# Kernel optimization log

Hardware: AMD Instinct MI355X
Metric: run time of the kernel (lower is better)

## Reference

```python
import jax, jax.numpy as jnp
import numpy as np

N_NODES = 100000
N_EDGES = 1600000
N_GRAPHS = 256
DIMS = [128, 128, 128, 128]  # gcn_layers_dim -> 3 GCNConv layers


def setup_inputs() -> dict:
    key = jax.random.key(0)
    ks = jax.random.split(key, 12)
    inp = {
        "x": jax.random.normal(ks[0], (N_NODES, DIMS[0]), jnp.float32),
        "edge_index": jax.random.randint(ks[1], (2, N_EDGES), 0, N_NODES),
        "edge_weight": jax.random.uniform(ks[2], (N_EDGES,), jnp.float32),
        "batch": jnp.sort(jax.random.randint(ks[3], (N_NODES,), 0, N_GRAPHS)),
    }
    for i in range(3):
        fan_in = DIMS[i]
        scale = 1.0 / np.sqrt(fan_in)
        inp[f"W{i+1}"] = jax.random.uniform(ks[4 + 2 * i], (DIMS[i], DIMS[i + 1]),
                                             jnp.float32, -scale, scale)
        inp[f"b{i+1}"] = jax.random.uniform(ks[5 + 2 * i], (DIMS[i + 1],),
                                             jnp.float32, -scale, scale)
    return inp


def reference(x, edge_index, edge_weight, batch, W1, b1, W2, b2, W3, b3):
    n = x.shape[0]
    # PyG GCNConv: add self-loops with weight 1, symmetric normalization.
    loop = jnp.arange(n)
    row = jnp.concatenate([edge_index[0], loop])  # source nodes
    col = jnp.concatenate([edge_index[1], loop])  # target nodes (aggregation index)
    w = jnp.concatenate([edge_weight, jnp.ones((n,), x.dtype)])
    deg = jax.ops.segment_sum(w, col, num_segments=n)
    dinv = jnp.where(deg > 0, jax.lax.rsqrt(deg), jnp.zeros_like(deg))
    norm = dinv[row] * w * dinv[col]  # [E+N]

    # global_mean_pool setup
    counts = jax.ops.segment_sum(jnp.ones((n,), x.dtype), batch,
                                 num_segments=N_GRAPHS)
    counts = jnp.maximum(counts, 1.0)[:, None]

    def gcn_conv(h, W, b):
        hl = h @ W                      # linear projection first (PyG order)
        msg = hl[row] * norm[:, None]   # gather + edge scaling
        out = jax.ops.segment_sum(msg, col, num_segments=n)  # scatter-add
        return out + b

    embeddings = []
    h = x
    for W, b in ((W1, b1), (W2, b2), (W3, b3)):
        h = gcn_conv(h, W, b)
        h = jax.nn.relu(h)              # relu_layers_index = [0,1,2]
        emb = jax.ops.segment_sum(h, batch, num_segments=N_GRAPHS) / counts
        embeddings.append(emb)          # gep = global_mean_pool
    return tuple(embeddings)
```

## Files before the change

kernel.cpp:

```cpp
#include <hip/hip_runtime.h>


typedef short short8 __attribute__((ext_vector_type(8)));
typedef float f32x4  __attribute__((ext_vector_type(4)));

__device__ inline unsigned pack_bf16x2(float a, float b) {
    unsigned ua = __float_as_uint(a);
    ua = (ua + 0x7FFFu + ((ua >> 16) & 1u)) >> 16;
    unsigned ub = __float_as_uint(b);
    ub = (ub + 0x7FFFu + ((ub >> 16) & 1u)) >> 16;
    return ua | (ub << 16);
}
__device__ inline ushort bf16_1(float a) {
    unsigned ua = __float_as_uint(a);
    return (ushort)((ua + 0x7FFFu + ((ua >> 16) & 1u)) >> 16);
}
__device__ inline float bf_lo(unsigned u) { return __uint_as_float(u << 16); }
__device__ inline float bf_hi(unsigned u) { return __uint_as_float(u & 0xFFFF0000u); }


template <bool F32IN>
__device__ __forceinline__ void gemm_tile(const void* __restrict__ Hin,
                                          const ushort* __restrict__ WbT,
                                          unsigned* __restrict__ O, int M,
                                          int bid, unsigned* sOut) {
    int lane = threadIdx.x & 63;
    int wv = threadIdx.x >> 6;
    int quad = lane >> 4;
    int mrow = lane & 15;
    int m0 = bid * 128 + wv * 32;
    int r0 = m0 + mrow;
    int r1 = r0 + 16;
    int r0c = r0 < M ? r0 : M - 1;
    int r1c = r1 < M ? r1 : M - 1;

    short8 a0[4], a1[4];
    if (F32IN) {
        const float* Hf = (const float*)Hin;
#pragma unroll
        for (int s = 0; s < 4; s++) {
            const float4* p0 = (const float4*)(Hf + (size_t)r0c * 128 + s * 32 + quad * 8);
            const float4* p1 = (const float4*)(Hf + (size_t)r1c * 128 + s * 32 + quad * 8);
            float4 f0 = p0[0], f1 = p0[1];
            float4 g0 = p1[0], g1 = p1[1];
            union { short8 s8; unsigned u[4]; } t0, t1;
            t0.u[0] = pack_bf16x2(f0.x, f0.y); t0.u[1] = pack_bf16x2(f0.z, f0.w);
            t0.u[2] = pack_bf16x2(f1.x, f1.y); t0.u[3] = pack_bf16x2(f1.z, f1.w);
            t1.u[0] = pack_bf16x2(g0.x, g0.y); t1.u[1] = pack_bf16x2(g0.z, g0.w);
            t1.u[2] = pack_bf16x2(g1.x, g1.y); t1.u[3] = pack_bf16x2(g1.z, g1.w);
            a0[s] = t0.s8; a1[s] = t1.s8;
        }
    } else {
        const unsigned* Hb = (const unsigned*)Hin;
#pragma unroll
        for (int s = 0; s < 4; s++) {
            a0[s] = *(const short8*)(Hb + (size_t)r0c * 64 + s * 16 + quad * 4);
            a1[s] = *(const short8*)(Hb + (size_t)r1c * 64 + s * 16 + quad * 4);
        }
    }
    f32x4 acc0[8], acc1[8];
#pragma unroll
    for (int t = 0; t < 8; t++) {
        acc0[t] = (f32x4){0.f, 0.f, 0.f, 0.f};
        acc1[t] = (f32x4){0.f, 0.f, 0.f, 0.f};
    }
#pragma unroll
    for (int s = 0; s < 4; s++) {
#pragma unroll
        for (int t = 0; t < 8; t++) {
            short8 b = *(const short8*)(WbT + (t * 16 + mrow) * 128 + s * 32 + quad * 8);
            acc0[t] = __builtin_amdgcn_mfma_f32_16x16x32_bf16(a0[s], b, acc0[t], 0, 0, 0);
            acc1[t] = __builtin_amdgcn_mfma_f32_16x16x32_bf16(a1[s], b, acc1[t], 0, 0, 0);
        }
    }
    ushort* so = (ushort*)(sOut + wv * 32 * 64);
#pragma unroll
    for (int t = 0; t < 8; t++) {
#pragma unroll
        for (int r = 0; r < 4; r++) {
            int lr = quad * 4 + r;
            int c = t * 16 + mrow;
            so[lr * 128 + c] = bf16_1(acc0[t][r]);
            so[(lr + 16) * 128 + c] = bf16_1(acc1[t][r]);
        }
    }
    __syncthreads();
    const unsigned* si = sOut + wv * 32 * 64;
#pragma unroll 8
    for (int r = 0; r < 32; r++) {
        int row = m0 + r;
        if (row < M) O[(size_t)row * 64 + lane] = si[r * 64 + lane];
    }
}

__device__ __forceinline__ void pool_tile(const unsigned* __restrict__ HB,
                                          const int* __restrict__ gb,
                                          float* __restrict__ outp, int g,
                                          float* part) {
    int lane = threadIdx.x & 63, w = threadIdx.x >> 6;
    int s = gb[g], e = gb[g + 1];
    float ax = 0.f, ay = 0.f;
    for (int i = s + w; i < e; i += 4) {
        unsigned u = HB[(size_t)i * 64 + lane];
        ax += bf_lo(u); ay += bf_hi(u);
    }
    part[w * 128 + lane * 2] = ax;
    part[w * 128 + lane * 2 + 1] = ay;
    __syncthreads();
    if (threadIdx.x < 128) {
        float sum = part[threadIdx.x] + part[128 + threadIdx.x]
                  + part[256 + threadIdx.x] + part[384 + threadIdx.x];
        float c = (float)(e - s);
        outp[g * 128 + threadIdx.x] = sum / fmaxf(c, 1.0f);
    }
}


__global__ void k_prep(int* __restrict__ cnt, int N, int* __restrict__ bsum,
                       const int* __restrict__ batch, int* __restrict__ gb, int G,
                       const float* __restrict__ W0, const float* __restrict__ W1,
                       const float* __restrict__ W2, ushort* __restrict__ WbT) {
    int id = blockIdx.x * blockDim.x + threadIdx.x;
    if (id < N) cnt[id] = 0;
    if (id < 128) bsum[id] = 0;
    if (id <= G) {
        int lo = 0, hi = N;
        while (lo < hi) { int mid = (lo + hi) >> 1; if (batch[mid] < id) lo = mid + 1; else hi = mid; }
        gb[id] = lo;
    }
    if (id < 3 * 16384) {
        int l = id >> 14;
        const float* W = (l == 0) ? W0 : ((l == 1) ? W1 : W2);
        int id2 = id & 16383;
        int n = id2 & 127, k = id2 >> 7;
        WbT[l * 16384 + n * 128 + k] = bf16_1(W[k * 128 + n]);
    }
}

__global__ __launch_bounds__(256) void k_phase1(const int* __restrict__ ei,
                                                int* __restrict__ cnt,
                                                int* __restrict__ epos, int E,
                                                const float* __restrict__ x,
                                                const ushort* __restrict__ WbT,
                                                unsigned* __restrict__ O, int M,
                                                int nbGemm) {
    __shared__ unsigned sBuf[8192];
    if (blockIdx.x < nbGemm) {
        gemm_tile<true>(x, WbT, O, M, blockIdx.x, sBuf);
        return;
    }
    int tid = (blockIdx.x - nbGemm) * 256 + threadIdx.x;
    if (tid < E) {
        int c = ei[E + tid];
        epos[tid] = atomicAdd(&cnt[c], 1);
    }
}

__global__ __launch_bounds__(1024) void k_scan1(const int* __restrict__ cnt,
                                                int* __restrict__ pre,
                                                int* __restrict__ bsum, int n) {
    __shared__ int wsum[16];
    int t = threadIdx.x, lane = t & 63, w = t >> 6;
    int i = blockIdx.x * 1024 + t;
    int v = (i < n) ? cnt[i] : 0;
    int x = v;
#pragma unroll
    for (int off = 1; off < 64; off <<= 1) {
        int y = __shfl_up(x, off, 64);
        if (lane >= off) x += y;
    }
    if (lane == 63) wsum[w] = x;
    __syncthreads();
    int woff = 0, tot = 0;
#pragma unroll
    for (int q = 0; q < 16; q++) { int s = wsum[q]; if (q < w) woff += s; tot += s; }
    if (i < n) pre[i] = woff + x - v;
    if (t == 0) bsum[blockIdx.x] = tot;
}

__global__ __launch_bounds__(256) void k_scatter(const int* __restrict__ ei,
                                                 const float* __restrict__ ew,
                                                 const int* __restrict__ pre,
                                                 const int* __restrict__ bsumRaw,
                                                 int* __restrict__ ptrv,
                                                 const int* __restrict__ epos,
                                                 int2* __restrict__ csr, int E, int N) {
    __shared__ int sRaw[256];
    __shared__ int sPre[256];
    __shared__ int sWt[4];
    int t = threadIdx.x;
    sRaw[t] = (t < 128) ? bsumRaw[t] : 0;
    __syncthreads();
    int lane = t & 63, w2 = t >> 6;
    int v = sRaw[t];
    int x = v;
#pragma unroll
    for (int off = 1; off < 64; off <<= 1) {
        int y = __shfl_up(x, off, 64);
        if (lane >= off) x += y;
    }
    if (lane == 63) sWt[w2] = x;
    __syncthreads();
    int base = 0;
#pragma unroll
    for (int q = 0; q < 4; q++) { if (q < w2) base += sWt[q]; }
    sPre[t] = base + x - v;
    __syncthreads();
    int e = blockIdx.x * 256 + t;
    if (e < N) ptrv[e] = pre[e] + sPre[e >> 10];
    if (e == 0) ptrv[N] = sWt[0] + sWt[1];
    if (e >= E) return;
    int r = ei[e];
    int c = ei[E + e];
    int2 mv; mv.x = r; mv.y = __float_as_int(ew[e]);
    csr[pre[c] + sPre[c >> 10] + epos[e]] = mv;
}

__global__ __launch_bounds__(256) void k_degdinv(const int2* __restrict__ csr,
                                                 const int* __restrict__ ptrv,
                                                 float* __restrict__ dinv, int N) {
    int node = blockIdx.x * 8 + (threadIdx.x >> 5);
    int j = threadIdx.x & 31;
    if (node >= N) return;
    int e0 = ptrv[node], e1 = ptrv[node + 1];
    float s = (j == 0) ? 1.0f : 0.0f;
    for (int e = e0 + j; e < e1; e += 32) s += __int_as_float(csr[e].y);
#pragma unroll
    for (int off = 1; off < 32; off <<= 1) s += __shfl_xor(s, off, 64);
    if (j == 0) dinv[node] = rsqrtf(s);
}

__global__ __launch_bounds__(256) void k_norm(int2* __restrict__ csr,
                                              const int* __restrict__ ptrv,
                                              const float* __restrict__ dinv, int N) {
    int node = blockIdx.x * 8 + (threadIdx.x >> 5);
    int j = threadIdx.x & 31;
    if (node >= N) return;
    float dc = dinv[node];
    int e0 = ptrv[node], e1 = ptrv[node + 1];
    for (int e = e0 + j; e < e1; e += 32) {
        int2 m = csr[e];
        m.y = __float_as_int(dinv[m.x] * __int_as_float(m.y) * dc);
        csr[e] = m;
    }
}

__global__ __launch_bounds__(256) void k_agg(const unsigned* __restrict__ HL,
                                             const int* __restrict__ ptr,
                                             const int2* __restrict__ csr,
                                             const float* __restrict__ dinv,
                                             const float* __restrict__ bias,
                                             unsigned* __restrict__ Hout, int M) {
    __shared__ int2 sM[4 * 64];
    int node = (int)((blockIdx.x * blockDim.x + threadIdx.x) >> 6);
    if (node >= M) return;
    int lane = threadIdx.x & 63;
    int half = lane >> 5;
    int q = lane & 31;
    int2* mbase = &sM[(threadIdx.x >> 6) * 64];
    int e0 = ptr[node], e1 = ptr[node + 1];
    int deg = e1 - e0;
    int nbv = deg < 64 ? deg : 64;
    if (lane < nbv) mbase[lane] = csr[e0 + lane];
    const uint2* HL2 = (const uint2*)HL;
    float di = dinv[node];
    float sn = (half == 0) ? di * di : 0.f;
    uint2 us = HL2[(size_t)node * 32 + q];
    float a0 = sn * bf_lo(us.x), a1 = sn * bf_hi(us.x);
    float a2 = sn * bf_lo(us.y), a3 = sn * bf_hi(us.y);
    int j = half;
    for (; j + 8 <= nbv; j += 8) {
        int2 m[4]; uint2 u[4];
#pragma unroll
        for (int t = 0; t < 4; t++) m[t] = mbase[j + 2 * t];
#pragma unroll
        for (int t = 0; t < 4; t++) u[t] = HL2[(size_t)m[t].x * 32 + q];
#pragma unroll
        for (int t = 0; t < 4; t++) {
            float nv = __int_as_float(m[t].y);
            a0 += nv * bf_lo(u[t].x); a1 += nv * bf_hi(u[t].x);
            a2 += nv * bf_lo(u[t].y); a3 += nv * bf_hi(u[t].y);
        }
    }
    for (; j < nbv; j += 2) {
        int2 m = mbase[j];
        uint2 u = HL2[(size_t)m.x * 32 + q];
        float nv = __int_as_float(m.y);
        a0 += nv * bf_lo(u.x); a1 += nv * bf_hi(u.x);
        a2 += nv * bf_lo(u.y); a3 += nv * bf_hi(u.y);
    }
    for (int e = e0 + 64 + half; e < e1; e += 2) {
        int2 m = csr[e];
        uint2 u = HL2[(size_t)m.x * 32 + q];
        float nv = __int_as_float(m.y);
        a0 += nv * bf_lo(u.x); a1 += nv * bf_hi(u.x);
        a2 += nv * bf_lo(u.y); a3 += nv * bf_hi(u.y);
    }
    a0 += __shfl_xor(a0, 32, 64);
    a1 += __shfl_xor(a1, 32, 64);
    a2 += __shfl_xor(a2, 32, 64);
    a3 += __shfl_xor(a3, 32, 64);
    float4 bv = ((const float4*)bias)[q];
    float r0 = fmaxf(a0 + bv.x, 0.f);
    float r1 = fmaxf(a1 + bv.y, 0.f);
    float r2 = fmaxf(a2 + bv.z, 0.f);
    float r3 = fmaxf(a3 + bv.w, 0.f);
    if (half == 0) {
        uint2 pv;
        pv.x = pack_bf16x2(r0, r1);
        pv.y = pack_bf16x2(r2, r3);
        ((uint2*)(Hout + (size_t)node * 64))[q] = pv;
    }
}

__global__ __launch_bounds__(256) void k_gemm_pool(const unsigned* __restrict__ Hb,
                                                   const ushort* __restrict__ WbT,
                                                   unsigned* __restrict__ O, int M,
                                                   const int* __restrict__ gb,
                                                   float* __restrict__ outp,
                                                   int nbGemm) {
    __shared__ unsigned sBuf[8192];
    if (blockIdx.x < nbGemm) {
        gemm_tile<false>(Hb, WbT, O, M, blockIdx.x, sBuf);
        return;
    }
    pool_tile(Hb, gb, outp, blockIdx.x - nbGemm, (float*)sBuf);
}

extern "C" void kernel_launch(void* const* d_in, const int* in_sizes, int n_in,
                              void* d_out, int out_size, void* d_ws, size_t ws_size,
                              hipStream_t stream) {
    const float* x     = (const float*)d_in[0];
    const int*   ei    = (const int*)d_in[1];
    const float* ew    = (const float*)d_in[2];
    const int*   batch = (const int*)d_in[3];
    const float* Wt[3] = {(const float*)d_in[4], (const float*)d_in[6], (const float*)d_in[8]};
    const float* bt[3] = {(const float*)d_in[5], (const float*)d_in[7], (const float*)d_in[9]};
    float* out = (float*)d_out;

    const int D = 128;
    const int N = in_sizes[0] / D;
    const int E = in_sizes[2];
    const int G = out_size / (3 * D);

    char* p = (char*)d_ws;
    auto alloc = [&](size_t bytes) {
        void* r = (void*)p;
        p += (bytes + 255) & ~(size_t)255;
        return r;
    };
    int*      cnt    = (int*)alloc((size_t)N * 4);
    int*      ptr    = (int*)alloc((size_t)(N + 1) * 4);
    int*      pre    = (int*)alloc((size_t)N * 4);
    int*      bsum   = (int*)alloc((size_t)128 * 4);
    int*      gb     = (int*)alloc((size_t)(G + 1) * 4);
    float*    dinv   = (float*)alloc((size_t)N * 4);
    ushort*   WbT    = (ushort*)alloc((size_t)3 * 16384 * 2);
    int2*     csr    = (int2*)alloc((size_t)E * 8);
    unsigned* bufHL  = (unsigned*)alloc((size_t)N * 64 * 4);
    unsigned* bufH   = (unsigned*)alloc((size_t)N * 64 * 4);
    int*      epos   = (int*)bufH;

    int nb = (N + 1023) / 1024;
    int nbGemm = (N + 127) / 128;
    int nbAtomic = (E + 255) / 256;
    int prepWork = N > 3 * 16384 ? N : 3 * 16384;

    k_prep<<<(prepWork + 255) / 256, 256, 0, stream>>>(cnt, N, bsum, batch, gb, G,
                                                       Wt[0], Wt[1], Wt[2], WbT);
    k_phase1<<<nbGemm + nbAtomic, 256, 0, stream>>>(ei, cnt, epos, E,
                                                    x, WbT, bufHL, N, nbGemm);
    k_scan1<<<nb, 1024, 0, stream>>>(cnt, pre, bsum, N);
    k_scatter<<<(E + 255) / 256, 256, 0, stream>>>(ei, ew, pre, bsum, ptr, epos,
                                                   csr, E, N);
    k_degdinv<<<(N + 7) / 8, 256, 0, stream>>>(csr, ptr, dinv, N);
    k_norm<<<(N + 7) / 8, 256, 0, stream>>>(csr, ptr, dinv, N);

    k_agg<<<(N + 3) / 4, 256, 0, stream>>>(bufHL, ptr, csr, dinv, bt[0], bufH, N);
    k_gemm_pool<<<nbGemm + G, 256, 0, stream>>>(bufH, WbT + 16384, bufHL, N,
                                                gb, out + 0 * (size_t)G * D, nbGemm);
    k_agg<<<(N + 3) / 4, 256, 0, stream>>>(bufHL, ptr, csr, dinv, bt[1], bufH, N);
    k_gemm_pool<<<nbGemm + G, 256, 0, stream>>>(bufH, WbT + 2 * 16384, bufHL, N,
                                                gb, out + 1 * (size_t)G * D, nbGemm);
    k_agg<<<(N + 3) / 4, 256, 0, stream>>>(bufHL, ptr, csr, dinv, bt[2], bufH, N);
    k_gemm_pool<<<G, 256, 0, stream>>>(bufH, WbT, nullptr, 0,
                                       gb, out + 2 * (size_t)G * D, 0);
}
```

Before: 564.3 us.

## Fuse degree sum into count atomics via packed 64-bit fixed-point counters

Edge counting and weighted degree accumulation are merged into one 64-bit atomic per edge: the count sits in the high bits and a fixed-point edge weight in the low bits. The scan kernel then computes dinv directly, and the scatter kernel computes the normalized weight inline while taking its slot with a second atomic cursor. This removes the separate degree and normalization passes over the CSR. Each counter gets its own cache line to cut atomic contention. The trade-offs are a quantized degree sum (weights rounded to 22 fractional bits), an extra atomic per edge during scatter, and a nondeterministic edge order within each CSR row.

```diff
diff --git a/kernel.cpp b/kernel.cpp
--- a/kernel.cpp
+++ b/kernel.cpp
@@ -116,12 +116,13 @@
 }
 
 
-__global__ void k_prep(int* __restrict__ cnt, int N, int* __restrict__ bsum,
+__global__ void k_prep(unsigned long long* __restrict__ lines, int N,
+                       int* __restrict__ bsum,
                        const int* __restrict__ batch, int* __restrict__ gb, int G,
                        const float* __restrict__ W0, const float* __restrict__ W1,
                        const float* __restrict__ W2, ushort* __restrict__ WbT) {
     int id = blockIdx.x * blockDim.x + threadIdx.x;
-    if (id < N) cnt[id] = 0;
+    if (id < N) lines[(size_t)id * 8] = 0ULL;
     if (id < 128) bsum[id] = 0;
     if (id <= G) {
         int lo = 0, hi = N;
@@ -138,8 +139,9 @@
 }
 
 __global__ __launch_bounds__(256) void k_phase1(const int* __restrict__ ei,
-                                                int* __restrict__ cnt,
-                                                int* __restrict__ epos, int E,
+                                                const float* __restrict__ ew,
+                                                unsigned long long* __restrict__ lines,
+                                                int E,
                                                 const float* __restrict__ x,
                                                 const ushort* __restrict__ WbT,
                                                 unsigned* __restrict__ O, int M,
@@ -149,20 +151,33 @@
         gemm_tile<true>(x, WbT, O, M, blockIdx.x, sBuf);
         return;
     }
-    int tid = (blockIdx.x - nbGemm) * 256 + threadIdx.x;
-    if (tid < E) {
-        int c = ei[E + tid];
-        epos[tid] = atomicAdd(&cnt[c], 1);
-    }
-}
-
-__global__ __launch_bounds__(1024) void k_scan1(const int* __restrict__ cnt,
+    int base = (blockIdx.x - nbGemm) * 1024 + threadIdx.x;
+#pragma unroll
+    for (int q = 0; q < 4; q++) {
+        int e = base + q * 256;
+        if (e < E) {
+            int c = ei[E + e];
+            float w = ew[e];
+            unsigned long long pkt =
+                (1ULL << 40) | (unsigned long long)(unsigned)(w * 4194304.0f + 0.5f);
+            atomicAdd(&lines[(size_t)c * 8], pkt);
+        }
+    }
+}
+
+__global__ __launch_bounds__(1024) void k_scan1(unsigned long long* __restrict__ lines,
                                                 int* __restrict__ pre,
-                                                int* __restrict__ bsum, int n) {
+                                                int* __restrict__ bsum,
+                                                float* __restrict__ dinv, int n) {
     __shared__ int wsum[16];
     int t = threadIdx.x, lane = t & 63, w = t >> 6;
     int i = blockIdx.x * 1024 + t;
-    int v = (i < n) ? cnt[i] : 0;
+    int v = 0; float dg = 1.0f;
+    if (i < n) {
+        unsigned long long u = lines[(size_t)i * 8];
+        v = (int)(u >> 40);
+        dg = 1.0f + (float)(u & 0xFFFFFFFFFFULL) * (1.0f / 4194304.0f);
+    }
     int x = v;
 #pragma unroll
     for (int off = 1; off < 64; off <<= 1) {
@@ -174,7 +189,12 @@
     int woff = 0, tot = 0;
 #pragma unroll
     for (int q = 0; q < 16; q++) { int s = wsum[q]; if (q < w) woff += s; tot += s; }
-    if (i < n) pre[i] = woff + x - v;
+    if (i < n) {
+        int ex = woff + x - v;
+        pre[i] = ex;
+        ((int*)lines)[(size_t)i * 16] = ex;
+        dinv[i] = rsqrtf(dg);
+    }
     if (t == 0) bsum[blockIdx.x] = tot;
 }
 
@@ -183,7 +203,8 @@
                                                  const int* __restrict__ pre,
                                                  const int* __restrict__ bsumRaw,
                                                  int* __restrict__ ptrv,
-                                                 const int* __restrict__ epos,
+                                                 const float* __restrict__ dinv,
+                                                 int* __restrict__ cur,
                                                  int2* __restrict__ csr, int E, int N) {
     __shared__ int sRaw[256];
     __shared__ int sPre[256];
@@ -212,37 +233,10 @@
     if (e >= E) return;
     int r = ei[e];
     int c = ei[E + e];
-    int2 mv; mv.x = r; mv.y = __float_as_int(ew[e]);
-    csr[pre[c] + sPre[c >> 10] + epos[e]] = mv;
-}
-
-__global__ __launch_bounds__(256) void k_degdinv(const int2* __restrict__ csr,
-                                                 const int* __restrict__ ptrv,
-                                                 float* __restrict__ dinv, int N) {
-    int node = blockIdx.x * 8 + (threadIdx.x >> 5);
-    int j = threadIdx.x & 31;
-    if (node >= N) return;
-    int e0 = ptrv[node], e1 = ptrv[node + 1];
-    float s = (j == 0) ? 1.0f : 0.0f;
-    for (int e = e0 + j; e < e1; e += 32) s += __int_as_float(csr[e].y);
-#pragma unroll
-    for (int off = 1; off < 32; off <<= 1) s += __shfl_xor(s, off, 64);
-    if (j == 0) dinv[node] = rsqrtf(s);
-}
-
-__global__ __launch_bounds__(256) void k_norm(int2* __restrict__ csr,
-                                              const int* __restrict__ ptrv,
-                                              const float* __restrict__ dinv, int N) {
-    int node = blockIdx.x * 8 + (threadIdx.x >> 5);
-    int j = threadIdx.x & 31;
-    if (node >= N) return;
-    float dc = dinv[node];
-    int e0 = ptrv[node], e1 = ptrv[node + 1];
-    for (int e = e0 + j; e < e1; e += 32) {
-        int2 m = csr[e];
-        m.y = __float_as_int(dinv[m.x] * __int_as_float(m.y) * dc);
-        csr[e] = m;
-    }
+    float y = dinv[r] * ew[e] * dinv[c];
+    int slot = sPre[c >> 10] + atomicAdd(&cur[(size_t)c * 16], 1);
+    int2 mv; mv.x = r; mv.y = __float_as_int(y);
+    csr[slot] = mv;
 }
 
 __global__ __launch_bounds__(256) void k_agg(const unsigned* __restrict__ HL,
@@ -349,7 +343,6 @@
         p += (bytes + 255) & ~(size_t)255;
         return r;
     };
-    int*      cnt    = (int*)alloc((size_t)N * 4);
     int*      ptr    = (int*)alloc((size_t)(N + 1) * 4);
     int*      pre    = (int*)alloc((size_t)N * 4);
     int*      bsum   = (int*)alloc((size_t)128 * 4);
@@ -359,22 +352,20 @@
     int2*     csr    = (int2*)alloc((size_t)E * 8);
     unsigned* bufHL  = (unsigned*)alloc((size_t)N * 64 * 4);
     unsigned* bufH   = (unsigned*)alloc((size_t)N * 64 * 4);
-    int*      epos   = (int*)bufH;
+    unsigned long long* lines = (unsigned long long*)bufH;
 
     int nb = (N + 1023) / 1024;
     int nbGemm = (N + 127) / 128;
-    int nbAtomic = (E + 255) / 256;
+    int nbAtomic = (E + 1023) / 1024;
     int prepWork = N > 3 * 16384 ? N : 3 * 16384;
 
-    k_prep<<<(prepWork + 255) / 256, 256, 0, stream>>>(cnt, N, bsum, batch, gb, G,
+    k_prep<<<(prepWork + 255) / 256, 256, 0, stream>>>(lines, N, bsum, batch, gb, G,
                                                        Wt[0], Wt[1], Wt[2], WbT);
-    k_phase1<<<nbGemm + nbAtomic, 256, 0, stream>>>(ei, cnt, epos, E,
+    k_phase1<<<nbGemm + nbAtomic, 256, 0, stream>>>(ei, ew, lines, E,
                                                     x, WbT, bufHL, N, nbGemm);
-    k_scan1<<<nb, 1024, 0, stream>>>(cnt, pre, bsum, N);
-    k_scatter<<<(E + 255) / 256, 256, 0, stream>>>(ei, ew, pre, bsum, ptr, epos,
-                                                   csr, E, N);
-    k_degdinv<<<(N + 7) / 8, 256, 0, stream>>>(csr, ptr, dinv, N);
-    k_norm<<<(N + 7) / 8, 256, 0, stream>>>(csr, ptr, dinv, N);
+    k_scan1<<<nb, 1024, 0, stream>>>(lines, pre, bsum, dinv, N);
+    k_scatter<<<(E + 255) / 256, 256, 0, stream>>>(ei, ew, pre, bsum, ptr, dinv,
+                                                   (int*)lines, csr, E, N);
 
     k_agg<<<(N + 3) / 4, 256, 0, stream>>>(bufHL, ptr, csr, dinv, bt[0], bufH, N);
     k_gemm_pool<<<nbGemm + G, 256, 0, stream>>>(bufH, WbT + 16384, bufHL, N,
```

Measured after the change: 586.3 us. 3.9% more time.
